# Performance work log

Hardware: AMD Instinct MI355X
Metric: run time of the kernel (lower is better)

Reference implementation:

```python
import jax, jax.numpy as jnp
import numpy as np

E = 250000   # n_scanned_edges
B = 16       # batch_size
N = 50000    # n_entities (n_nodes)
R = 500      # n_relations
D_IN = 100   # input embedding dim (proj input)
D = 64       # n_dims_sm
M = 2 * E    # n_memorized_and_scanned_nodes (>= n_vi_groups + n_vj_groups)


def setup_inputs() -> dict:
    rng = np.random.default_rng(0)
    eg = rng.integers(0, B, E)
    vi = rng.integers(0, N, E)
    vj = rng.integers(0, N, E)
    order = np.lexsort((vj, vi, eg))  # sorted by (eg_idx, vi, vj) as the module assumes
    eg, vi, vj = eg[order], vi[order], vj[order]
    rel = rng.integers(0, R, E)
    # dense group ids; idx_vi is non-decreasing because edges are lexsorted by (eg,vi)
    idx_vi = np.unique(eg.astype(np.int64) * N + vi, return_inverse=True)[1]
    idx_vj = np.unique(eg.astype(np.int64) * N + vj, return_inverse=True)[1]
    n_vi = int(idx_vi.max()) + 1
    edges = np.stack([eg, vi, vj, rel, idx_vi, idx_vj, idx_vi, n_vi + idx_vj], 1).astype(np.int32)

    key = jax.random.key(0)
    ks = jax.random.split(key, 24)
    nrm = lambda k, shp, s=1.0: jax.random.normal(k, shp, jnp.float32) * s
    na = jax.random.uniform(ks[0], (B, N), jnp.float32)
    na = na / jnp.sum(na, 1, keepdims=True)  # node attention is a distribution per example
    inp = {
        "node_attention": na,
        "scanned_edges": jnp.asarray(edges),
        "hidden_uncon": nrm(ks[1], (1, N, D_IN)),
        "hidden_con": nrm(ks[2], (M, D_IN)),
        "rel_table": nrm(ks[3], (R, D_IN)),
        "query_head_emb": nrm(ks[4], (B, D_IN)),
        "query_rel_emb": nrm(ks[5], (B, D_IN)),
        "p_W": nrm(ks[6], (D_IN, D), 0.1),
        "p_b": jnp.zeros((D,), jnp.float32),
    }
    i = 7
    for g in ("g1", "g2"):
        for nm, shp in (("lW", (4 * D, D)), ("lb", (D,)), ("rW", (4 * D, D)), ("rb", (D,)), ("cW", (D, D)), ("cb", (D,))):
            inp[g + "_" + nm] = nrm(ks[i], shp, 0.05)
            i += 1
    return inp


def _g(left, right, lW, lb, rW, rb, cW, cb):
    # G layer: sum(left_dense(cat(left)) * center_dense(right_dense(cat(right))), -1)
    lx = jnp.concatenate(left, -1)
    rx = jnp.concatenate(right, -1)
    l = jax.nn.leaky_relu(lx @ lW + lb, 0.2)  # tf.nn.leaky_relu alpha=0.2
    r = jax.nn.leaky_relu(rx @ rW + rb, 0.2)
    return jnp.sum(l * (r @ cW + cb), -1)


def reference(node_attention, scanned_edges, hidden_uncon, hidden_con, rel_table,
              query_head_emb, query_rel_emb, p_W, p_b,
              g1_lW, g1_lb, g1_rW, g1_rb, g1_cW, g1_cb,
              g2_lW, g2_lb, g2_rW, g2_rb, g2_cW, g2_cb):
    Bn, Nn = node_attention.shape
    En = scanned_edges.shape[0]
    proj = lambda x: jnp.tanh(x @ p_W + p_b)

    h_con = proj(hidden_con)       # (M, D)
    h_uncon = proj(hidden_uncon)   # (1, N, D)
    qh = proj(query_head_emb)      # (B, D)
    qr = proj(query_rel_emb)

    e = scanned_edges
    eg, vi, vj = e[:, 0], e[:, 1], e[:, 2]
    idx_vi = e[:, 4]
    # node2edge gathers
    h_vi = h_con[e[:, 6]]          # (E, D)
    h_vj = h_con[e[:, 7]]
    hu_vj = h_uncon[0][vj]         # hidden_uncon batch is 1 -> idx 0
    remb = proj(rel_table[e[:, 3]])
    qhv = qh[eg]
    qrv = qr[eg]

    left = (h_vi, remb, qhv, qrv)
    logits = _g(left, (h_vj, remb, qhv, qrv), g1_lW, g1_lb, g1_rW, g1_rb, g1_cW, g1_cb)
    logits = logits + _g(left, (hu_vj, remb, qhv, qrv), g2_lW, g2_lb, g2_rW, g2_rb, g2_cW, g2_cb)

    # neighbor softmax over sorted idx_vi segments
    m = jax.ops.segment_max(logits, idx_vi, num_segments=En, indices_are_sorted=True)
    ex = jnp.exp(logits - m[idx_vi])
    den = jax.ops.segment_sum(ex, idx_vi, num_segments=En, indices_are_sorted=True)
    transition = ex / den[idx_vi]

    # flow attention: gather at (eg, vi), scatter-sum at (eg, vj)
    trans_att = node_attention[eg, vi] * transition
    new_att = jnp.zeros((Bn, Nn), node_attention.dtype).at[eg, vj].add(trans_att)
    new_att = new_att / jnp.sum(new_att, axis=1, keepdims=True)
    return new_att
```

## Files before the change

kernel.cpp:

```cpp
#include <hip/hip_runtime.h>

#define DIN 100
#define DD  64
#define NE  250000
#define NB  16
#define NN  50000
#define NR  500
#define NM  500000
#define NH  (NM + NN)

#define H_OFF    64
#define TA2_OFF  (H_OFF + NH*DD)
#define RT_OFF   (TA2_OFF + NE*DD)
#define QT_OFF   (RT_OFF + 4*NR*DD)
#define LG_OFF   (QT_OFF + 4*NB*DD)

#define PA 475
#define PB 238
#define PC 55

__device__ __forceinline__ void fma4x4(const float4 x, const float4 w, float4 acc[4]) {
  acc[0].x += x.x*w.x; acc[0].y += x.x*w.y; acc[0].z += x.x*w.z; acc[0].w += x.x*w.w;
  acc[1].x += x.y*w.x; acc[1].y += x.y*w.y; acc[1].z += x.y*w.z; acc[1].w += x.y*w.w;
  acc[2].x += x.z*w.x; acc[2].y += x.z*w.y; acc[2].z += x.z*w.z; acc[2].w += x.z*w.w;
  acc[3].x += x.w*w.x; acc[3].y += x.w*w.y; acc[3].z += x.w*w.z; acc[3].w += x.w*w.w;
}

__device__ __forceinline__ float fc(const float4& v, int i) {
  return ((const float*)&v)[i];
}

__device__ __forceinline__ float4 leaky4(float4 v) {
  v.x = v.x > 0.f ? v.x : 0.2f*v.x;
  v.y = v.y > 0.f ? v.y : 0.2f*v.y;
  v.z = v.z > 0.f ? v.z : 0.2f*v.z;
  v.w = v.w > 0.f ? v.w : 0.2f*v.w;
  return v;
}

__global__ void k_init(int* wsI, float* bsum) {
  if (threadIdx.x == 0) { wsI[0] = 0x7fffffff; wsI[1] = 0; }
  if (threadIdx.x < NB) bsum[threadIdx.x] = 0.f;
}

__global__ void k_limits(const int* __restrict__ edges, int* __restrict__ wsI) {
  int i = blockIdx.x * blockDim.x + threadIdx.x;
  int mn = 0x7fffffff, mx = -1;
  if (i < NE) { int v = edges[i*8 + 7]; mn = v; mx = v; }
  for (int off = 32; off > 0; off >>= 1) {
    mn = min(mn, __shfl_down(mn, off));
    mx = max(mx, __shfl_down(mx, off));
  }
  if ((threadIdx.x & 63) == 0) {
    atomicMin(&wsI[0], mn);
    atomicMax(&wsI[1], mx + 1);
  }
}

__global__ void k_tables(const float* __restrict__ rtab,
                         const float* __restrict__ qh, const float* __restrict__ qr,
                         const float* __restrict__ pW, const float* __restrict__ pb,
                         const float* __restrict__ g1_lW, const float* __restrict__ g1_lb,
                         const float* __restrict__ g1_rW, const float* __restrict__ g1_rb,
                         const float* __restrict__ g2_lW, const float* __restrict__ g2_lb,
                         const float* __restrict__ g2_rW, const float* __restrict__ g2_rb,
                         float* __restrict__ rT, float* __restrict__ qT) {
  __shared__ float xs[DIN], xs2[DIN], ps[DD], ps2[DD];
  const int d = threadIdx.x;
  const int blk = blockIdx.x;
  if (blk < NR) {
    for (int k = d; k < DIN; k += 64) xs[k] = rtab[blk*DIN + k];
    __syncthreads();
    float a = pb[d];
    for (int k = 0; k < DIN; ++k) a += xs[k] * pW[k*DD + d];
    ps[d] = tanhf(a);
    __syncthreads();
    float o1 = 0.f, o2 = 0.f, o3 = 0.f, o4 = 0.f;
    for (int k = 0; k < DD; ++k) {
      float p = ps[k];
      o1 += p * g1_lW[(DD + k)*DD + d];
      o2 += p * g1_rW[(DD + k)*DD + d];
      o3 += p * g2_lW[(DD + k)*DD + d];
      o4 += p * g2_rW[(DD + k)*DD + d];
    }
    rT[(0*NR + blk)*DD + d] = o1;
    rT[(1*NR + blk)*DD + d] = o2;
    rT[(2*NR + blk)*DD + d] = o3;
    rT[(3*NR + blk)*DD + d] = o4;
  } else {
    const int b = blk - NR;
    for (int k = d; k < DIN; k += 64) { xs[k] = qh[b*DIN + k]; xs2[k] = qr[b*DIN + k]; }
    __syncthreads();
    float a = pb[d], a2 = pb[d];
    for (int k = 0; k < DIN; ++k) { a += xs[k]*pW[k*DD + d]; a2 += xs2[k]*pW[k*DD + d]; }
    ps[d] = tanhf(a); ps2[d] = tanhf(a2);
    __syncthreads();
    float o1 = g1_lb[d], o2 = g1_rb[d], o3 = g2_lb[d], o4 = g2_rb[d];
    for (int k = 0; k < DD; ++k) {
      float p = ps[k], p2 = ps2[k];
      o1 += p * g1_lW[(2*DD + k)*DD + d] + p2 * g1_lW[(3*DD + k)*DD + d];
      o2 += p * g1_rW[(2*DD + k)*DD + d] + p2 * g1_rW[(3*DD + k)*DD + d];
      o3 += p * g2_lW[(2*DD + k)*DD + d] + p2 * g2_lW[(3*DD + k)*DD + d];
      o4 += p * g2_rW[(2*DD + k)*DD + d] + p2 * g2_rW[(3*DD + k)*DD + d];
    }
    qT[(0*NB + b)*DD + d] = o1;
    qT[(1*NB + b)*DD + d] = o2;
    qT[(2*NB + b)*DD + d] = o3;
    qT[(3*NB + b)*DD + d] = o4;
  }
}

__global__ __launch_bounds__(256, 3)
void k_proj(const float* __restrict__ hcon, const float* __restrict__ huncon,
            const float* __restrict__ pW, const float* __restrict__ pb,
            const int* __restrict__ lim, float* __restrict__ H) {
  __shared__ __align__(16) float pWs[DIN*DD];
  const int tid = threadIdx.x;
  for (int i = tid; i < DIN*DD; i += 256) pWs[i] = pW[i];
  const int tc = tid & 7, tr = tid >> 3;
  const int c0 = tc << 3;
  const float4 pb0 = *(const float4*)&pb[c0];
  const float4 pb1 = *(const float4*)&pb[c0 + 4];
  const int nmax = lim[1];
  const int t_lo = (nmax + 255) >> 8;
  const int NT   = t_lo + ((NN + 255) >> 8);
  __syncthreads();
  for (int t = blockIdx.x; t < NT; t += gridDim.x) {
    const bool lo = (t < t_lo);
    const int row0 = lo ? (t << 8) : (NM + ((t - t_lo) << 8));
    const int rlim = lo ? nmax : NH;
    const float* srcs[8];
    #pragma unroll
    for (int r = 0; r < 8; ++r) {
      int row = row0 + tr*8 + r;
      if (row >= rlim) row = rlim - 1;
      srcs[r] = lo ? &hcon[(size_t)row*DIN] : &huncon[(size_t)(row - NM)*DIN];
    }
    float4 acc[2][2][4];
    #pragma unroll
    for (int a = 0; a < 2; ++a)
      #pragma unroll
      for (int b = 0; b < 2; ++b)
        #pragma unroll
        for (int i = 0; i < 4; ++i) acc[a][b][i] = make_float4(0.f,0.f,0.f,0.f);
    for (int kb = 0; kb < DIN; kb += 4) {
      float4 xv[8];
      #pragma unroll
      for (int r = 0; r < 8; ++r) xv[r] = *(const float4*)(srcs[r] + kb);
      #pragma unroll
      for (int kk = 0; kk < 4; ++kk) {
        float4 w0 = *(const float4*)&pWs[(kb + kk)*DD + c0];
        float4 w1 = *(const float4*)&pWs[(kb + kk)*DD + c0 + 4];
        float4 xa = make_float4(fc(xv[0],kk), fc(xv[1],kk), fc(xv[2],kk), fc(xv[3],kk));
        float4 xb = make_float4(fc(xv[4],kk), fc(xv[5],kk), fc(xv[6],kk), fc(xv[7],kk));
        fma4x4(xa, w0, acc[0][0]); fma4x4(xa, w1, acc[0][1]);
        fma4x4(xb, w0, acc[1][0]); fma4x4(xb, w1, acc[1][1]);
      }
    }
    #pragma unroll
    for (int a = 0; a < 2; ++a)
      #pragma unroll
      for (int i = 0; i < 4; ++i) {
        int row = row0 + tr*8 + a*4 + i;
        if (row < rlim) {
          float4 o0, o1;
          o0.x = tanhf(acc[a][0][i].x + pb0.x);
          o0.y = tanhf(acc[a][0][i].y + pb0.y);
          o0.z = tanhf(acc[a][0][i].z + pb0.z);
          o0.w = tanhf(acc[a][0][i].w + pb0.w);
          o1.x = tanhf(acc[a][1][i].x + pb1.x);
          o1.y = tanhf(acc[a][1][i].y + pb1.y);
          o1.z = tanhf(acc[a][1][i].z + pb1.z);
          o1.w = tanhf(acc[a][1][i].w + pb1.w);
          *(float4*)&H[(size_t)row*DD + c0]     = o0;
          *(float4*)&H[(size_t)row*DD + c0 + 4] = o1;
        }
      }
  }
}

__device__ __forceinline__ void gemm64(const float* const* srcs, const float* __restrict__ Wss,
                                       int c0, float4 acc[2][2][4]) {
  #pragma unroll
  for (int a = 0; a < 2; ++a)
    #pragma unroll
    for (int b = 0; b < 2; ++b)
      #pragma unroll
      for (int i = 0; i < 4; ++i) acc[a][b][i] = make_float4(0.f,0.f,0.f,0.f);
  for (int kb = 0; kb < DD; kb += 4) {
    float4 xv[8];
    #pragma unroll
    for (int r = 0; r < 8; ++r) xv[r] = *(const float4*)(srcs[r] + kb);
    #pragma unroll
    for (int kk = 0; kk < 4; ++kk) {
      float4 w0 = *(const float4*)&Wss[(kb + kk)*DD + c0];
      float4 w1 = *(const float4*)&Wss[(kb + kk)*DD + c0 + 4];
      float4 xa = make_float4(fc(xv[0],kk), fc(xv[1],kk), fc(xv[2],kk), fc(xv[3],kk));
      float4 xb = make_float4(fc(xv[4],kk), fc(xv[5],kk), fc(xv[6],kk), fc(xv[7],kk));
      fma4x4(xa, w0, acc[0][0]); fma4x4(xa, w1, acc[0][1]);
      fma4x4(xb, w0, acc[1][0]); fma4x4(xb, w1, acc[1][1]);
    }
  }
}

__global__ __launch_bounds__(256, 3)
void k_tf(const float* __restrict__ g1_lW, const float* __restrict__ g1_rW,
          const float* __restrict__ g2_lW, const float* __restrict__ g2_rW,
          const int* __restrict__ lim,
          float* __restrict__ H, float* __restrict__ TA2) {
  __shared__ __align__(16) float Ws0[DD*DD];
  __shared__ __align__(16) float Ws1[DD*DD];
  const int tid = threadIdx.x;
  const int nvi  = lim[0];
  const int nmax = lim[1];
  int pool, pbase, pgrid;
  if (blockIdx.x < PA)           { pool = 0; pbase = blockIdx.x;           pgrid = PA; }
  else if (blockIdx.x < PA + PB) { pool = 1; pbase = blockIdx.x - PA;      pgrid = PB; }
  else                           { pool = 2; pbase = blockIdx.x - PA - PB; pgrid = PC; }
  if (pool == 0) {
    for (int i = tid; i < DD*DD; i += 256) { Ws0[i] = g1_lW[i]; Ws1[i] = g2_lW[i]; }
  } else if (pool == 1) {
    for (int i = tid; i < DD*DD; i += 256) Ws0[i] = g1_rW[i];
  } else {
    for (int i = tid; i < DD*DD; i += 256) Ws0[i] = g2_rW[i];
  }
  int t_begin, t_count, row_base, rlim, wlo, whi;
  if (pool == 0)      { t_begin = 0;        t_count = (nvi + 255) >> 8;                 row_base = 0;  rlim = nmax; wlo = 0;   whi = nvi;  }
  else if (pool == 1) { t_begin = nvi >> 8; t_count = ((nmax + 255) >> 8) - (nvi >> 8); row_base = 0;  rlim = nmax; wlo = nvi; whi = nmax; }
  else                { t_begin = 0;        t_count = (NN + 255) >> 8;                  row_base = NM; rlim = NH;   wlo = NM;  whi = NH;   }
  const int tc = tid & 7, tr = tid >> 3;
  const int c0 = tc << 3;
  __syncthreads();
  for (int tt = pbase; tt < t_count; tt += pgrid) {
    const int row0 = row_base + ((t_begin + tt) << 8);
    const float* srcs[8];
    #pragma unroll
    for (int r = 0; r < 8; ++r) {
      int row = row0 + tr*8 + r;
      if (row >= rlim) row = rlim - 1;
      srcs[r] = &H[(size_t)row*DD];
    }
    float4 acc[2][2][4];
    if (pool == 0) {
      gemm64(srcs, Ws1, c0, acc);
      #pragma unroll
      for (int a = 0; a < 2; ++a)
        #pragma unroll
        for (int i = 0; i < 4; ++i) {
          int row = row0 + tr*8 + a*4 + i;
          if (row >= wlo && row < whi) {
            *(float4*)&TA2[(size_t)row*DD + c0]     = acc[a][0][i];
            *(float4*)&TA2[(size_t)row*DD + c0 + 4] = acc[a][1][i];
          }
        }
    }
    gemm64(srcs, Ws0, c0, acc);
    __syncthreads();
    #pragma unroll
    for (int a = 0; a < 2; ++a)
      #pragma unroll
      for (int i = 0; i < 4; ++i) {
        int row = row0 + tr*8 + a*4 + i;
        if (row >= wlo && row < whi) {
          *(float4*)&H[(size_t)row*DD + c0]     = acc[a][0][i];
          *(float4*)&H[(size_t)row*DD + c0 + 4] = acc[a][1][i];
        }
      }
  }
}

__global__ __launch_bounds__(256, 2)
void k_edges(const int* __restrict__ edges,
             const float* __restrict__ TA, const float* __restrict__ TA2,
             const float* __restrict__ HU2,
             const float* __restrict__ rT, const float* __restrict__ qT,
             const float* __restrict__ cW1, const float* __restrict__ cb1,
             const float* __restrict__ cW2, const float* __restrict__ cb2,
             float* __restrict__ logits) {
  __shared__ __align__(16) float Wt1s[DD*68];
  __shared__ __align__(16) float Wt2s[DD*68];
  __shared__ __align__(16) float Lt[DD][68];
  __shared__ __align__(16) float Rt[DD][68];
  __shared__ __align__(16) float4 cbs4[2][16];
  __shared__ float lg[64];
  __shared__ int   se[64*8];
  const int tid = threadIdx.x;
  for (int i = tid; i < DD*DD; i += 256) {
    int k = i >> 6, d = i & 63;
    Wt1s[d*68 + k] = cW1[i];
    Wt2s[d*68 + k] = cW2[i];
  }
  if (tid < 16) {
    cbs4[0][tid] = *(const float4*)&cb1[tid*4];
    cbs4[1][tid] = *(const float4*)&cb2[tid*4];
  }
  const int e   = tid >> 2;
  const int d0  = (tid & 3) * 16;
  const int eq0 = (tid >> 4) << 2;
  const int jq0 = (tid & 15) << 2;
  __syncthreads();
  const int NT = (NE + 63) / 64;
  for (int tile = blockIdx.x; tile < NT; tile += gridDim.x) {
    const int e0 = tile * 64;
    const int ecnt = min(64, NE - e0);
    for (int i = tid; i < 64*8; i += 256) se[i] = (i < ecnt*8) ? edges[e0*8 + i] : 0;
    if (tid < 64) lg[tid] = 0.f;
    __syncthreads();
    const int rel = se[e*8 + 3];
    const int eg  = se[e*8 + 0];
    const int li  = se[e*8 + 6];
    for (int g = 0; g < 2; ++g) {
      const float* Lb = g ? TA2 : TA;
      const float* Rb = g ? HU2 : TA;
      const float* rL = rT + (g ? 2*NR*DD : 0);
      const float* rR = rT + (g ? 3*NR*DD : 1*NR*DD);
      const float* qL = qT + (g ? 2*NB*DD : 0);
      const float* qR = qT + (g ? 3*NB*DD : 1*NB*DD);
      const float* Wts = g ? Wt2s : Wt1s;
      const int ri = g ? se[e*8 + 2] : se[e*8 + 7];
      float cbp = 0.f;
      #pragma unroll
      for (int di = 0; di < 4; ++di) {
        const int d = d0 + 4*di;
        float4 l = *(const float4*)&Lb[(size_t)li*DD + d];
        float4 t = *(const float4*)&rL[rel*DD + d];
        float4 u = *(const float4*)&qL[eg*DD + d];
        l.x += t.x + u.x; l.y += t.y + u.y; l.z += t.z + u.z; l.w += t.w + u.w;
        l = leaky4(l);
        Lt[d+0][e] = l.x; Lt[d+1][e] = l.y; Lt[d+2][e] = l.z; Lt[d+3][e] = l.w;
        float4 c = cbs4[g][d >> 2];
        cbp += l.x*c.x + l.y*c.y + l.z*c.z + l.w*c.w;
        float4 r = *(const float4*)&Rb[(size_t)ri*DD + d];
        t = *(const float4*)&rR[rel*DD + d];
        u = *(const float4*)&qR[eg*DD + d];
        r.x += t.x + u.x; r.y += t.y + u.y; r.z += t.z + u.z; r.w += t.w + u.w;
        r = leaky4(r);
        Rt[d+0][e] = r.x; Rt[d+1][e] = r.y; Rt[d+2][e] = r.z; Rt[d+3][e] = r.w;
      }
      atomicAdd(&lg[e], cbp);
      __syncthreads();
      float4 z[4] = {{0,0,0,0},{0,0,0,0},{0,0,0,0},{0,0,0,0}};
      for (int d = 0; d < DD; ++d) {
        float4 x = *(const float4*)&Lt[d][eq0];
        float4 w = *(const float4*)&Wts[d*68 + jq0];
        fma4x4(x, w, z);
      }
      float4 rv0 = *(const float4*)&Rt[jq0+0][eq0];
      float4 rv1 = *(const float4*)&Rt[jq0+1][eq0];
      float4 rv2 = *(const float4*)&Rt[jq0+2][eq0];
      float4 rv3 = *(const float4*)&Rt[jq0+3][eq0];
      float p0 = z[0].x*rv0.x + z[0].y*rv1.x + z[0].z*rv2.x + z[0].w*rv3.x;
      float p1 = z[1].x*rv0.y + z[1].y*rv1.y + z[1].z*rv2.y + z[1].w*rv3.y;
      float p2 = z[2].x*rv0.z + z[2].y*rv1.z + z[2].z*rv2.z + z[2].w*rv3.z;
      float p3 = z[3].x*rv0.w + z[3].y*rv1.w + z[3].z*rv2.w + z[3].w*rv3.w;
      #pragma unroll
      for (int m = 1; m < 16; m <<= 1) {
        p0 += __shfl_xor(p0, m);
        p1 += __shfl_xor(p1, m);
        p2 += __shfl_xor(p2, m);
        p3 += __shfl_xor(p3, m);
      }
      if ((tid & 15) == 0) {
        lg[eq0+0] += p0;
        lg[eq0+1] += p1;
        lg[eq0+2] += p2;
        lg[eq0+3] += p3;
      }
      __syncthreads();
    }
    if (tid < ecnt) logits[e0 + tid] = lg[tid];
    __syncthreads();
  }
}

__global__ void k_softmax(const int* __restrict__ edges, const float* __restrict__ logits,
                          const float* __restrict__ na, float* __restrict__ out) {
  int e = blockIdx.x * blockDim.x + threadIdx.x;
  if (e >= NE) return;
  int seg = edges[e*8 + 4];
  if (e > 0 && edges[(e-1)*8 + 4] == seg) return;
  int j = e;
  float m = -1e30f;
  while (j < NE && edges[j*8 + 4] == seg) { m = fmaxf(m, logits[j]); ++j; }
  float s = 0.f;
  for (int t = e; t < j; ++t) s += expf(logits[t] - m);
  int eg = edges[e*8 + 0], vi = edges[e*8 + 1];
  float scale = na[eg*NN + vi] / s;
  for (int t = e; t < j; ++t) {
    int vj = edges[t*8 + 2];
    __hip_atomic_fetch_add(&out[eg*NN + vj], expf(logits[t] - m) * scale,
                           __ATOMIC_RELAXED, __HIP_MEMORY_SCOPE_AGENT);
  }
}

__global__ void k_rowsum(const float* __restrict__ out, float* __restrict__ bsum) {
  int b = blockIdx.y;
  float s = 0.f;
  for (int n = blockIdx.x * blockDim.x + threadIdx.x; n < NN; n += gridDim.x * blockDim.x)
    s += out[b*NN + n];
  for (int off = 32; off > 0; off >>= 1) s += __shfl_down(s, off);
  if ((threadIdx.x & 63) == 0)
    __hip_atomic_fetch_add(&bsum[b], s, __ATOMIC_RELAXED, __HIP_MEMORY_SCOPE_AGENT);
}

__global__ void k_div(float* __restrict__ out, const float* __restrict__ bsum) {
  int i = blockIdx.x * blockDim.x + threadIdx.x;
  if (i < NB*NN) out[i] /= bsum[i / NN];
}

extern "C" void kernel_launch(void* const* d_in, const int* in_sizes, int n_in,
                              void* d_out, int out_size, void* d_ws, size_t ws_size,
                              hipStream_t stream) {
  (void)in_sizes; (void)n_in; (void)out_size; (void)ws_size;
  const float* na     = (const float*)d_in[0];
  const int*   edges  = (const int*)  d_in[1];
  const float* huncon = (const float*)d_in[2];
  const float* hcon   = (const float*)d_in[3];
  const float* rtab   = (const float*)d_in[4];
  const float* qh     = (const float*)d_in[5];
  const float* qr     = (const float*)d_in[6];
  const float* pW     = (const float*)d_in[7];
  const float* pb     = (const float*)d_in[8];
  const float* g1_lW  = (const float*)d_in[9];
  const float* g1_lb  = (const float*)d_in[10];
  const float* g1_rW  = (const float*)d_in[11];
  const float* g1_rb  = (const float*)d_in[12];
  const float* g1_cW  = (const float*)d_in[13];
  const float* g1_cb  = (const float*)d_in[14];
  const float* g2_lW  = (const float*)d_in[15];
  const float* g2_lb  = (const float*)d_in[16];
  const float* g2_rW  = (const float*)d_in[17];
  const float* g2_rb  = (const float*)d_in[18];
  const float* g2_cW  = (const float*)d_in[19];
  const float* g2_cb  = (const float*)d_in[20];
  float* out  = (float*)d_out;
  float* ws   = (float*)d_ws;
  int*   wsI  = (int*)d_ws;
  float* bsum = ws + 16;
  float* H    = ws + H_OFF;
  float* TA2  = ws + TA2_OFF;
  float* rT   = ws + RT_OFF;
  float* qT   = ws + QT_OFF;
  float* lgp  = ws + LG_OFF;

  hipMemsetAsync(d_out, 0, (size_t)NB*NN*sizeof(float), stream);
  k_init<<<1, 64, 0, stream>>>(wsI, bsum);
  k_limits<<<(NE + 255)/256, 256, 0, stream>>>(edges, wsI);
  k_tables<<<NR + NB, 64, 0, stream>>>(rtab, qh, qr, pW, pb,
                                       g1_lW, g1_lb, g1_rW, g1_rb,
                                       g2_lW, g2_lb, g2_rW, g2_rb, rT, qT);
  k_proj<<<768, 256, 0, stream>>>(hcon, huncon, pW, pb, wsI, H);
  k_tf<<<PA + PB + PC, 256, 0, stream>>>(g1_lW, g1_rW, g2_lW, g2_rW, wsI, H, TA2);
  k_edges<<<512, 256, 0, stream>>>(edges, H, TA2, H + NM*DD, rT, qT,
                                   g1_cW, g1_cb, g2_cW, g2_cb, lgp);
  k_softmax<<<(NE + 255)/256, 256, 0, stream>>>(edges, lgp, na, out);
  k_rowsum<<<dim3(32, 16), 256, 0, stream>>>(out, bsum);
  k_div<<<(NB*NN + 255)/256, 256, 0, stream>>>(out, bsum);
}
```

Measured before the change: 860.4 us.

## Fuse projection and per-node G transforms into one tiled kernel via shared memory

Merges the k_proj projection kernel and the k_tf G-layer transform kernel into a single kernel that processes 128-row tiles. Each tile is staged transposed in LDS, projected with tanh, written back to LDS, and then multiplied by the G weights without a round trip of the intermediate H through global memory. The weights are now read straight from global/L1 instead of LDS, and the pool block counts change. This removes one launch and the HBM write and read of the projected embeddings, at the cost of extra barriers and uncached weight loads.

```diff
diff --git a/kernel.cpp b/kernel.cpp
--- a/kernel.cpp
+++ b/kernel.cpp
@@ -15,9 +15,11 @@
 #define QT_OFF   (RT_OFF + 4*NR*DD)
 #define LG_OFF   (QT_OFF + 4*NB*DD)
 
-#define PA 475
-#define PB 238
-#define PC 55
+#define PA 408
+#define PB 292
+#define PC 68
+
+#define US 132
 
 __device__ __forceinline__ void fma4x4(const float4 x, const float4 w, float4 acc[4]) {
   acc[0].x += x.x*w.x; acc[0].y += x.x*w.y; acc[0].z += x.x*w.z; acc[0].w += x.x*w.w;
@@ -111,105 +113,13 @@
 }
 
 __global__ __launch_bounds__(256, 3)
-void k_proj(const float* __restrict__ hcon, const float* __restrict__ huncon,
-            const float* __restrict__ pW, const float* __restrict__ pb,
-            const int* __restrict__ lim, float* __restrict__ H) {
-  __shared__ __align__(16) float pWs[DIN*DD];
-  const int tid = threadIdx.x;
-  for (int i = tid; i < DIN*DD; i += 256) pWs[i] = pW[i];
-  const int tc = tid & 7, tr = tid >> 3;
-  const int c0 = tc << 3;
-  const float4 pb0 = *(const float4*)&pb[c0];
-  const float4 pb1 = *(const float4*)&pb[c0 + 4];
-  const int nmax = lim[1];
-  const int t_lo = (nmax + 255) >> 8;
-  const int NT   = t_lo + ((NN + 255) >> 8);
-  __syncthreads();
-  for (int t = blockIdx.x; t < NT; t += gridDim.x) {
-    const bool lo = (t < t_lo);
-    const int row0 = lo ? (t << 8) : (NM + ((t - t_lo) << 8));
-    const int rlim = lo ? nmax : NH;
-    const float* srcs[8];
-    #pragma unroll
-    for (int r = 0; r < 8; ++r) {
-      int row = row0 + tr*8 + r;
-      if (row >= rlim) row = rlim - 1;
-      srcs[r] = lo ? &hcon[(size_t)row*DIN] : &huncon[(size_t)(row - NM)*DIN];
-    }
-    float4 acc[2][2][4];
-    #pragma unroll
-    for (int a = 0; a < 2; ++a)
-      #pragma unroll
-      for (int b = 0; b < 2; ++b)
-        #pragma unroll
-        for (int i = 0; i < 4; ++i) acc[a][b][i] = make_float4(0.f,0.f,0.f,0.f);
-    for (int kb = 0; kb < DIN; kb += 4) {
-      float4 xv[8];
-      #pragma unroll
-      for (int r = 0; r < 8; ++r) xv[r] = *(const float4*)(srcs[r] + kb);
-      #pragma unroll
-      for (int kk = 0; kk < 4; ++kk) {
-        float4 w0 = *(const float4*)&pWs[(kb + kk)*DD + c0];
-        float4 w1 = *(const float4*)&pWs[(kb + kk)*DD + c0 + 4];
-        float4 xa = make_float4(fc(xv[0],kk), fc(xv[1],kk), fc(xv[2],kk), fc(xv[3],kk));
-        float4 xb = make_float4(fc(xv[4],kk), fc(xv[5],kk), fc(xv[6],kk), fc(xv[7],kk));
-        fma4x4(xa, w0, acc[0][0]); fma4x4(xa, w1, acc[0][1]);
-        fma4x4(xb, w0, acc[1][0]); fma4x4(xb, w1, acc[1][1]);
-      }
-    }
-    #pragma unroll
-    for (int a = 0; a < 2; ++a)
-      #pragma unroll
-      for (int i = 0; i < 4; ++i) {
-        int row = row0 + tr*8 + a*4 + i;
-        if (row < rlim) {
-          float4 o0, o1;
-          o0.x = tanhf(acc[a][0][i].x + pb0.x);
-          o0.y = tanhf(acc[a][0][i].y + pb0.y);
-          o0.z = tanhf(acc[a][0][i].z + pb0.z);
-          o0.w = tanhf(acc[a][0][i].w + pb0.w);
-          o1.x = tanhf(acc[a][1][i].x + pb1.x);
-          o1.y = tanhf(acc[a][1][i].y + pb1.y);
-          o1.z = tanhf(acc[a][1][i].z + pb1.z);
-          o1.w = tanhf(acc[a][1][i].w + pb1.w);
-          *(float4*)&H[(size_t)row*DD + c0]     = o0;
-          *(float4*)&H[(size_t)row*DD + c0 + 4] = o1;
-        }
-      }
-  }
-}
-
-__device__ __forceinline__ void gemm64(const float* const* srcs, const float* __restrict__ Wss,
-                                       int c0, float4 acc[2][2][4]) {
-  #pragma unroll
-  for (int a = 0; a < 2; ++a)
-    #pragma unroll
-    for (int b = 0; b < 2; ++b)
-      #pragma unroll
-      for (int i = 0; i < 4; ++i) acc[a][b][i] = make_float4(0.f,0.f,0.f,0.f);
-  for (int kb = 0; kb < DD; kb += 4) {
-    float4 xv[8];
-    #pragma unroll
-    for (int r = 0; r < 8; ++r) xv[r] = *(const float4*)(srcs[r] + kb);
-    #pragma unroll
-    for (int kk = 0; kk < 4; ++kk) {
-      float4 w0 = *(const float4*)&Wss[(kb + kk)*DD + c0];
-      float4 w1 = *(const float4*)&Wss[(kb + kk)*DD + c0 + 4];
-      float4 xa = make_float4(fc(xv[0],kk), fc(xv[1],kk), fc(xv[2],kk), fc(xv[3],kk));
-      float4 xb = make_float4(fc(xv[4],kk), fc(xv[5],kk), fc(xv[6],kk), fc(xv[7],kk));
-      fma4x4(xa, w0, acc[0][0]); fma4x4(xa, w1, acc[0][1]);
-      fma4x4(xb, w0, acc[1][0]); fma4x4(xb, w1, acc[1][1]);
-    }
-  }
-}
-
-__global__ __launch_bounds__(256, 3)
-void k_tf(const float* __restrict__ g1_lW, const float* __restrict__ g1_rW,
-          const float* __restrict__ g2_lW, const float* __restrict__ g2_rW,
-          const int* __restrict__ lim,
-          float* __restrict__ H, float* __restrict__ TA2) {
-  __shared__ __align__(16) float Ws0[DD*DD];
-  __shared__ __align__(16) float Ws1[DD*DD];
+void k_projtf(const float* __restrict__ hcon, const float* __restrict__ huncon,
+              const float* __restrict__ pW, const float* __restrict__ pb,
+              const float* __restrict__ g1_lW, const float* __restrict__ g1_rW,
+              const float* __restrict__ g2_lW, const float* __restrict__ g2_rW,
+              const int* __restrict__ lim,
+              float* __restrict__ H, float* __restrict__ TA2) {
+  __shared__ __align__(16) float U[DIN*US];
   const int tid = threadIdx.x;
   const int nvi  = lim[0];
   const int nmax = lim[1];
@@ -217,55 +127,122 @@
   if (blockIdx.x < PA)           { pool = 0; pbase = blockIdx.x;           pgrid = PA; }
   else if (blockIdx.x < PA + PB) { pool = 1; pbase = blockIdx.x - PA;      pgrid = PB; }
   else                           { pool = 2; pbase = blockIdx.x - PA - PB; pgrid = PC; }
+  int t_begin, t_count, row_base, rlim, wlo, whi;
+  const float* Xsrc;
+  const float* W0;
+  const float* W1 = nullptr;
   if (pool == 0) {
-    for (int i = tid; i < DD*DD; i += 256) { Ws0[i] = g1_lW[i]; Ws1[i] = g2_lW[i]; }
+    t_begin = 0; t_count = (nvi + 127) >> 7; row_base = 0; rlim = nmax;
+    wlo = 0; whi = nvi; Xsrc = hcon; W0 = g1_lW; W1 = g2_lW;
   } else if (pool == 1) {
-    for (int i = tid; i < DD*DD; i += 256) Ws0[i] = g1_rW[i];
+    t_begin = nvi >> 7; t_count = ((nmax + 127) >> 7) - (nvi >> 7); row_base = 0; rlim = nmax;
+    wlo = nvi; whi = nmax; Xsrc = hcon; W0 = g1_rW;
   } else {
-    for (int i = tid; i < DD*DD; i += 256) Ws0[i] = g2_rW[i];
-  }
-  int t_begin, t_count, row_base, rlim, wlo, whi;
-  if (pool == 0)      { t_begin = 0;        t_count = (nvi + 255) >> 8;                 row_base = 0;  rlim = nmax; wlo = 0;   whi = nvi;  }
-  else if (pool == 1) { t_begin = nvi >> 8; t_count = ((nmax + 255) >> 8) - (nvi >> 8); row_base = 0;  rlim = nmax; wlo = nvi; whi = nmax; }
-  else                { t_begin = 0;        t_count = (NN + 255) >> 8;                  row_base = NM; rlim = NH;   wlo = NM;  whi = NH;   }
+    t_begin = 0; t_count = (NN + 127) >> 7; row_base = NM; rlim = NH;
+    wlo = NM; whi = NH; Xsrc = huncon; W0 = g2_rW;
+  }
   const int tc = tid & 7, tr = tid >> 3;
   const int c0 = tc << 3;
-  __syncthreads();
+  const int r0 = tr << 2;
+  const float4 pb0 = *(const float4*)&pb[c0];
+  const float4 pb1 = *(const float4*)&pb[c0 + 4];
+  const int srow = tid >> 1;
+  const int kbeg = (tid & 1) ? 48 : 0;
+  const int kcnt = (tid & 1) ? 52 : 48;
+
   for (int tt = pbase; tt < t_count; tt += pgrid) {
-    const int row0 = row_base + ((t_begin + tt) << 8);
-    const float* srcs[8];
+    const int row0 = row_base + ((t_begin + tt) << 7);
+    {
+      int row = row0 + srow;
+      if (row >= rlim) row = rlim - 1;
+      const float* src = Xsrc + (size_t)(row - row_base)*DIN + kbeg;
+      #pragma unroll
+      for (int j = 0; j < 52; j += 4) {
+        if (j < kcnt) {
+          float4 v = *(const float4*)(src + j);
+          U[(kbeg+j+0)*US + srow] = v.x;
+          U[(kbeg+j+1)*US + srow] = v.y;
+          U[(kbeg+j+2)*US + srow] = v.z;
+          U[(kbeg+j+3)*US + srow] = v.w;
+        }
+      }
+    }
+    __syncthreads();
+    float4 ap0[4] = {{0,0,0,0},{0,0,0,0},{0,0,0,0},{0,0,0,0}};
+    float4 ap1[4] = {{0,0,0,0},{0,0,0,0},{0,0,0,0},{0,0,0,0}};
+    #pragma unroll 4
+    for (int k = 0; k < DIN; ++k) {
+      float4 x  = *(const float4*)&U[k*US + r0];
+      float4 w0 = *(const float4*)&pW[k*DD + c0];
+      float4 w1 = *(const float4*)&pW[k*DD + c0 + 4];
+      fma4x4(x, w0, ap0);
+      fma4x4(x, w1, ap1);
+    }
+    __syncthreads();
     #pragma unroll
-    for (int r = 0; r < 8; ++r) {
-      int row = row0 + tr*8 + r;
-      if (row >= rlim) row = rlim - 1;
-      srcs[r] = &H[(size_t)row*DD];
-    }
-    float4 acc[2][2][4];
+    for (int c = 0; c < 4; ++c) {
+      float4 hv;
+      hv.x = tanhf(fc(ap0[0], c) + fc(pb0, c));
+      hv.y = tanhf(fc(ap0[1], c) + fc(pb0, c));
+      hv.z = tanhf(fc(ap0[2], c) + fc(pb0, c));
+      hv.w = tanhf(fc(ap0[3], c) + fc(pb0, c));
+      *(float4*)&U[(c0 + c)*US + r0] = hv;
+    }
+    #pragma unroll
+    for (int c = 0; c < 4; ++c) {
+      float4 hv;
+      hv.x = tanhf(fc(ap1[0], c) + fc(pb1, c));
+      hv.y = tanhf(fc(ap1[1], c) + fc(pb1, c));
+      hv.z = tanhf(fc(ap1[2], c) + fc(pb1, c));
+      hv.w = tanhf(fc(ap1[3], c) + fc(pb1, c));
+      *(float4*)&U[(c0 + 4 + c)*US + r0] = hv;
+    }
+    __syncthreads();
     if (pool == 0) {
-      gemm64(srcs, Ws1, c0, acc);
+      float4 t0a[4] = {{0,0,0,0},{0,0,0,0},{0,0,0,0},{0,0,0,0}};
+      float4 t0b[4] = {{0,0,0,0},{0,0,0,0},{0,0,0,0},{0,0,0,0}};
+      float4 t1a[4] = {{0,0,0,0},{0,0,0,0},{0,0,0,0},{0,0,0,0}};
+      float4 t1b[4] = {{0,0,0,0},{0,0,0,0},{0,0,0,0},{0,0,0,0}};
+      #pragma unroll 4
+      for (int k = 0; k < DD; ++k) {
+        float4 x  = *(const float4*)&U[k*US + r0];
+        float4 w0 = *(const float4*)&W0[k*DD + c0];
+        float4 w1 = *(const float4*)&W0[k*DD + c0 + 4];
+        float4 u0 = *(const float4*)&W1[k*DD + c0];
+        float4 u1 = *(const float4*)&W1[k*DD + c0 + 4];
+        fma4x4(x, w0, t0a); fma4x4(x, w1, t0b);
+        fma4x4(x, u0, t1a); fma4x4(x, u1, t1b);
+      }
       #pragma unroll
-      for (int a = 0; a < 2; ++a)
-        #pragma unroll
-        for (int i = 0; i < 4; ++i) {
-          int row = row0 + tr*8 + a*4 + i;
-          if (row >= wlo && row < whi) {
-            *(float4*)&TA2[(size_t)row*DD + c0]     = acc[a][0][i];
-            *(float4*)&TA2[(size_t)row*DD + c0 + 4] = acc[a][1][i];
-          }
+      for (int r = 0; r < 4; ++r) {
+        int row = row0 + r0 + r;
+        if (row >= wlo && row < whi) {
+          *(float4*)&H[(size_t)row*DD + c0]       = t0a[r];
+          *(float4*)&H[(size_t)row*DD + c0 + 4]   = t0b[r];
+          *(float4*)&TA2[(size_t)row*DD + c0]     = t1a[r];
+          *(float4*)&TA2[(size_t)row*DD + c0 + 4] = t1b[r];
         }
-    }
-    gemm64(srcs, Ws0, c0, acc);
-    __syncthreads();
-    #pragma unroll
-    for (int a = 0; a < 2; ++a)
+      }
+    } else {
+      float4 t0a[4] = {{0,0,0,0},{0,0,0,0},{0,0,0,0},{0,0,0,0}};
+      float4 t0b[4] = {{0,0,0,0},{0,0,0,0},{0,0,0,0},{0,0,0,0}};
+      #pragma unroll 4
+      for (int k = 0; k < DD; ++k) {
+        float4 x  = *(const float4*)&U[k*US + r0];
+        float4 w0 = *(const float4*)&W0[k*DD + c0];
+        float4 w1 = *(const float4*)&W0[k*DD + c0 + 4];
+        fma4x4(x, w0, t0a); fma4x4(x, w1, t0b);
+      }
       #pragma unroll
-      for (int i = 0; i < 4; ++i) {
-        int row = row0 + tr*8 + a*4 + i;
+      for (int r = 0; r < 4; ++r) {
+        int row = row0 + r0 + r;
         if (row >= wlo && row < whi) {
-          *(float4*)&H[(size_t)row*DD + c0]     = acc[a][0][i];
-          *(float4*)&H[(size_t)row*DD + c0 + 4] = acc[a][1][i];
+          *(float4*)&H[(size_t)row*DD + c0]     = t0a[r];
+          *(float4*)&H[(size_t)row*DD + c0 + 4] = t0b[r];
         }
       }
+    }
+    __syncthreads();
   }
 }
 
@@ -449,8 +426,9 @@
   k_tables<<<NR + NB, 64, 0, stream>>>(rtab, qh, qr, pW, pb,
                                        g1_lW, g1_lb, g1_rW, g1_rb,
                                        g2_lW, g2_lb, g2_rW, g2_rb, rT, qT);
-  k_proj<<<768, 256, 0, stream>>>(hcon, huncon, pW, pb, wsI, H);
-  k_tf<<<PA + PB + PC, 256, 0, stream>>>(g1_lW, g1_rW, g2_lW, g2_rW, wsI, H, TA2);
+  k_projtf<<<PA + PB + PC, 256, 0, stream>>>(hcon, huncon, pW, pb,
+                                             g1_lW, g1_rW, g2_lW, g2_rW,
+                                             wsI, H, TA2);
   k_edges<<<512, 256, 0, stream>>>(edges, H, TA2, H + NM*DD, rT, qT,
                                    g1_cW, g1_cb, g2_cW, g2_cb, lgp);
   k_softmax<<<(NE + 255)/256, 256, 0, stream>>>(edges, lgp, na, out);
```

Measured after the change: 817.6 us. -5.0%, faster.
